# Performance work log

Hardware: AMD Instinct MI355X
Metric: run time of the kernel (lower is better)

## Reference

```python
import jax, jax.numpy as jnp
import numpy as np

TOL_A = 1e-09


def setup_inputs() -> dict:
    key = jax.random.key(0)
    ks = jax.random.split(key, 6)
    nx, nu, ny, bsz, T = 256, 128, 128, 128, 2048
    return {
        "u": jax.random.normal(ks[0], (bsz, T, nu), jnp.float32),
        "M": jax.random.normal(ks[1], (2 * nx, 2 * nx), jnp.float32),
        "B": jax.random.normal(ks[2], (nx, nu), jnp.float32),
        "C": jax.random.normal(ks[3], (ny, nx), jnp.float32),
        "D": jax.random.normal(ks[4], (ny, nu), jnp.float32),
        "x0": jax.random.normal(ks[5], (nx, 1), jnp.float32),
    }


def _compute_A(M):
    # LMI-based stable A: S = M M^T + tol*I; A = E^{-1} F
    nx = M.shape[0] // 2
    S = M @ M.T + TOL_A * jnp.eye(2 * nx, dtype=M.dtype)
    F = S[nx:, :nx]
    P = S[nx:, nx:]
    E = 0.5 * (P + S[:nx, :nx])
    return jnp.linalg.solve(E, F)  # == inv(E) @ F


def reference(u, M, B, C, D, x0):
    # u: (bsz, T, nu); returns predictions (bsz, T, ny)
    nx = B.shape[0]
    A = _compute_A(M)  # time-invariant: computed once instead of per step
    bsz = u.shape[0]
    x = jnp.broadcast_to(x0[:, 0], (bsz, nx))  # learned x0 stacked over batch
    # t=0 output: C x0 + D u_0 (faithful to torch code)
    y0 = x @ C.T + u[:, 0] @ D.T

    def step(x, u_t):
        # x_{t+1} = A x_t + B u_t ; y_{t+1} = C x_{t+1} + D u_t (off-by-one D term, as in source)
        x = x @ A.T + u_t @ B.T
        y = x @ C.T + u_t @ D.T
        return x, y

    # scan over time: xs is (T-1, bsz, nu)
    _, ys = jax.lax.scan(step, x, jnp.swapaxes(u[:, :-1], 0, 1))
    preds = jnp.concatenate([y0[None], ys], axis=0)  # (T, bsz, ny)
    return jnp.swapaxes(preds, 0, 1)
```

## Files before the change

### kernel.cpp

```cpp
#include <hip/hip_runtime.h>

#define NX 256
#define NU 128
#define NY 128
#define BSZ 128
#define TT 2048
#define LCH 32
#define KCH 64

typedef _Float16 h8 __attribute__((ext_vector_type(8)));
typedef _Float16 h4 __attribute__((ext_vector_type(4)));
typedef float f4 __attribute__((ext_vector_type(4)));

__device__ __forceinline__ f4 mfma16(h8 a, h8 b, f4 c) {
  return __builtin_amdgcn_mfma_f32_16x16x32_f16(a, b, c, 0, 0, 0);
}
#define PIN(x) asm volatile("" : "+v"(x))

__device__ __forceinline__ int swz256(int row, int bc) { return row * 256 + (bc ^ ((row & 7) << 4)); }

__device__ __forceinline__ h8 cvt8(f4 lo, f4 hi) {
  h8 h;
#pragma unroll
  for (int j = 0; j < 4; ++j) { h[j] = (_Float16)lo[j]; h[j + 4] = (_Float16)hi[j]; }
  return h;
}
__device__ __forceinline__ h4 h4cvt(f4 v) {
  h4 h;
#pragma unroll
  for (int j = 0; j < 4; ++j) h[j] = (_Float16)v[j];
  return h;
}
__device__ __forceinline__ h8 h8zero() {
  h8 h;
#pragma unroll
  for (int j = 0; j < 8; ++j) h[j] = (_Float16)0.0f;
  return h;
}

__device__ __forceinline__ void mm_core(const float* __restrict__ a, const float* __restrict__ b,
                                        int Nb, int i0, int j0, int tid,
                                        float (*As)[32][65], float (*Bs)[64][33],
                                        float acc[2][2]) {
  const int ar = tid >> 4, ac = (tid & 15) * 4;
  const int br = tid >> 3, bc = (tid & 7) * 4;
  const int tx = tid & 15, ty = tid >> 4;
  f4 pa0 = *(const f4*)(a + (size_t)(i0 + ar) * 256 + ac);
  f4 pa1 = *(const f4*)(a + (size_t)(i0 + ar + 16) * 256 + ac);
  f4 pb0 = *(const f4*)(b + (size_t)br * Nb + j0 + bc);
  f4 pb1 = *(const f4*)(b + (size_t)(br + 32) * Nb + j0 + bc);
  for (int r4 = 0; r4 < 4; ++r4) {
    const int bs = r4 & 1;
#pragma unroll
    for (int m = 0; m < 4; ++m) {
      As[bs][ar][ac + m] = pa0[m];
      As[bs][ar + 16][ac + m] = pa1[m];
      Bs[bs][br][bc + m] = pb0[m];
      Bs[bs][br + 32][bc + m] = pb1[m];
    }
    if (r4 < 3) {
      int kk = (r4 + 1) * 64;
      pa0 = *(const f4*)(a + (size_t)(i0 + ar) * 256 + kk + ac);
      pa1 = *(const f4*)(a + (size_t)(i0 + ar + 16) * 256 + kk + ac);
      pb0 = *(const f4*)(b + (size_t)(kk + br) * Nb + j0 + bc);
      pb1 = *(const f4*)(b + (size_t)(kk + br + 32) * Nb + j0 + bc);
    }
    __syncthreads();
#pragma unroll 8
    for (int k = 0; k < 64; ++k) {
      float a0 = As[bs][ty * 2][k], a1 = As[bs][ty * 2 + 1][k];
      float b0 = Bs[bs][k][tx * 2], b1 = Bs[bs][k][tx * 2 + 1];
      acc[0][0] += a0 * b0; acc[0][1] += a0 * b1;
      acc[1][0] += a1 * b0; acc[1][1] += a1 * b1;
    }
  }
}

__global__ __launch_bounds__(256) void k_ef(const float* __restrict__ M, const float* __restrict__ B,
                                            const float* __restrict__ C, const float* __restrict__ D,
                                            const float* __restrict__ x0, const float* __restrict__ u,
                                            float* __restrict__ E, float* __restrict__ F,
                                            _Float16* __restrict__ B16, float* __restrict__ out) {
  const int tid = threadIdx.x;
  int z = blockIdx.x >> 6;
  if (z >= 2) {
    if (blockIdx.x < 192) {
      int idx = (blockIdx.x - 128) * 256 + tid;
      int b = idx >> 7, col = idx & 127;
      const float* crow = C + (size_t)col * 256;
      const float* drow = D + (size_t)col * 128;
      const float* ur = u + (size_t)b * (TT * NU);
      float s = 0.f;
#pragma unroll 8
      for (int j = 0; j < 256; j += 4) {
        f4 cv = *(const f4*)(crow + j);
        f4 xv = *(const f4*)(x0 + j);
        s += cv[0] * xv[0] + cv[1] * xv[1] + cv[2] * xv[2] + cv[3] * xv[3];
      }
#pragma unroll 8
      for (int j = 0; j < 128; j += 4) {
        f4 dv = *(const f4*)(drow + j);
        f4 uv = *(const f4*)(ur + j);
        s += dv[0] * uv[0] + dv[1] * uv[1] + dv[2] * uv[2] + dv[3] * uv[3];
      }
      out[(size_t)b * (TT * NY) + col] = s;
    } else {
      int i = (blockIdx.x - 192) * 1024 + tid;
      B16[i] = (_Float16)B[i];
      B16[i + 256] = (_Float16)B[i + 256];
      B16[i + 512] = (_Float16)B[i + 512];
      B16[i + 768] = (_Float16)B[i + 768];
    }
    return;
  }
  __shared__ float Ps[2][32][65], Qs[2][32][65];
  int tile = blockIdx.x & 63;
  int i0 = (tile >> 3) * 32, j0 = (tile & 7) * 32;
  const int ar = tid >> 4, ac = (tid & 15) * 4;
  const int tx = tid & 15, ty = tid >> 4;
  float acc[2][2] = {{0.f, 0.f}, {0.f, 0.f}};
  int np = (z == 0) ? 2 : 1;
  int rc = 0;
  for (int p = 0; p < np; ++p) {
    int po = (z == 0) ? p * 256 : 256;
    int qo = (z == 0) ? p * 256 : 0;
    f4 p0 = *(const f4*)(M + (size_t)(i0 + po + ar) * 512 + ac);
    f4 p1 = *(const f4*)(M + (size_t)(i0 + po + ar + 16) * 512 + ac);
    f4 q0 = *(const f4*)(M + (size_t)(j0 + qo + ar) * 512 + ac);
    f4 q1 = *(const f4*)(M + (size_t)(j0 + qo + ar + 16) * 512 + ac);
    for (int kk = 0; kk < 512; kk += 64) {
      const int bs = rc & 1;
      ++rc;
#pragma unroll
      for (int m = 0; m < 4; ++m) {
        Ps[bs][ar][ac + m] = p0[m];
        Ps[bs][ar + 16][ac + m] = p1[m];
        Qs[bs][ar][ac + m] = q0[m];
        Qs[bs][ar + 16][ac + m] = q1[m];
      }
      if (kk < 448) {
        int k2 = kk + 64;
        p0 = *(const f4*)(M + (size_t)(i0 + po + ar) * 512 + k2 + ac);
        p1 = *(const f4*)(M + (size_t)(i0 + po + ar + 16) * 512 + k2 + ac);
        q0 = *(const f4*)(M + (size_t)(j0 + qo + ar) * 512 + k2 + ac);
        q1 = *(const f4*)(M + (size_t)(j0 + qo + ar + 16) * 512 + k2 + ac);
      }
      __syncthreads();
#pragma unroll 8
      for (int k = 0; k < 64; ++k) {
        float a0 = Ps[bs][ty * 2][k], a1 = Ps[bs][ty * 2 + 1][k];
        float b0 = Qs[bs][tx * 2][k], b1 = Qs[bs][tx * 2 + 1][k];
        acc[0][0] += a0 * b0; acc[0][1] += a0 * b1;
        acc[1][0] += a1 * b0; acc[1][1] += a1 * b1;
      }
    }
  }
#pragma unroll
  for (int ii = 0; ii < 2; ++ii)
#pragma unroll
    for (int jj = 0; jj < 2; ++jj) {
      int i = i0 + ty * 2 + ii, j = j0 + tx * 2 + jj;
      if (z == 0) {
        float v = 0.5f * acc[ii][jj];
        if (i == j) v += 1e-9f;
        E[i * 256 + j] = v;
      } else {
        F[i * 256 + j] = acc[ii][jj];
      }
    }
}

__global__ __launch_bounds__(256) void k_ns0(const float* __restrict__ E,
                                             float* __restrict__ X, float* __restrict__ Y) {
  __shared__ float As[2][32][65];
  __shared__ float Bs[2][64][33];
  __shared__ float s1[256], red[256];
  const int tid = threadIdx.x;
  {
    float s = 0.f;
    const float* row = E + (size_t)tid * 256;
#pragma unroll 8
    for (int j = 0; j < 256; j += 4) {
      f4 e = *(const f4*)(row + j);
      s += e[0] + e[1] + e[2] + e[3];
    }
    s1[tid] = s; red[tid] = s * s;
  }
  __syncthreads();
  for (int o = 128; o > 0; o >>= 1) { if (tid < o) red[tid] += red[tid + o]; __syncthreads(); }
  float n1 = red[0];
  __syncthreads();
  {
    float s = 0.f;
    const float* row = E + (size_t)tid * 256;
#pragma unroll 8
    for (int j = 0; j < 256; j += 4) {
      f4 e = *(const f4*)(row + j);
      f4 vv = *(const f4*)(&s1[j]);
      s += e[0] * vv[0] + e[1] * vv[1] + e[2] * vv[2] + e[3] * vv[3];
    }
    red[tid] = s * s;
  }
  __syncthreads();
  for (int o = 128; o > 0; o >>= 1) { if (tid < o) red[tid] += red[tid + o]; __syncthreads(); }
  float c = sqrtf(n1 / red[0]);
  __syncthreads();
  if (blockIdx.x < 64) {
    int i0 = (blockIdx.x >> 3) * 32, j0 = (blockIdx.x & 7) * 32;
    float acc[2][2] = {{0.f, 0.f}, {0.f, 0.f}};
    mm_core(E, E, 256, i0, j0, tid, As, Bs, acc);
    int tx = tid & 15, ty = tid >> 4;
#pragma unroll
    for (int ii = 0; ii < 2; ++ii)
#pragma unroll
      for (int jj = 0; jj < 2; ++jj) {
        int i = i0 + ty * 2 + ii, j = j0 + tx * 2 + jj;
        Y[(size_t)i * 256 + j] = 2.f * c * E[(size_t)i * 256 + j] - c * c * acc[ii][jj];
      }
  } else {
    int idx = (blockIdx.x - 64) * 1024 + tid * 4;
    int i = idx >> 8, j = idx & 255;
    f4 e = *(const f4*)(E + idx);
    f4 v;
#pragma unroll
    for (int m = 0; m < 4; ++m) v[m] = ((j + m) == i ? 2.f * c : 0.f) - c * c * e[m];
    *(f4*)(X + idx) = v;
  }
}

struct MMJob {
  const float* a; const float* b; const float* add;
  float* d32; _Float16* d16;
  int M, N, mode, blk0;
};

__global__ __launch_bounds__(256) void k_mm(MMJob j0, MMJob j1, MMJob j2, int njobs) {
  __shared__ float As[2][32][65];
  __shared__ float Bs[2][64][33];
  const int tid = threadIdx.x;
  int bid = blockIdx.x;
  MMJob jb = j0;
  if (njobs > 1 && bid >= j1.blk0) jb = j1;
  if (njobs > 2 && bid >= j2.blk0) jb = j2;
  int rel = bid - jb.blk0;
  int ntile = jb.N >> 5;
  int i0 = (rel / ntile) * 32, j0g = (rel % ntile) * 32;
  float acc[2][2] = {{0.f, 0.f}, {0.f, 0.f}};
  mm_core(jb.a, jb.b, jb.N, i0, j0g, tid, As, Bs, acc);
  int tx = tid & 15, ty = tid >> 4;
#pragma unroll
  for (int ii = 0; ii < 2; ++ii)
#pragma unroll
    for (int jj = 0; jj < 2; ++jj) {
      int i = i0 + ty * 2 + ii, j = j0g + tx * 2 + jj;
      size_t o = (size_t)i * jb.N + j;
      float v = acc[ii][jj];
      if (jb.mode == 1) v = 2.f * jb.a[(size_t)i * 256 + j] - v;
      else if (jb.add) v += jb.add[o];
      if (jb.d32) jb.d32[o] = v;
      if (jb.d16) jb.d16[o] = (_Float16)v;
    }
}

__global__ __launch_bounds__(512, 2) void k_recW(const float* __restrict__ u,
                                                 const _Float16* __restrict__ A16,
                                                 const _Float16* __restrict__ B16,
                                                 float* __restrict__ w) {
  __shared__ __align__(16) char sm[24576];
  char* xb = sm;
  char* ub = sm + 16384;
  const int tid = threadIdx.x, lane = tid & 63, wv = tid >> 6;
  const int g = lane >> 4, lr = lane & 15;
  const int chunk = blockIdx.x >> 3, btile = blockIdx.x & 7;
  const int b0 = btile * 16, t0 = chunk * LCH, nt0 = wv * 2;

  h8 Ar[2][8], Bf[2][4];
#pragma unroll
  for (int n2 = 0; n2 < 2; ++n2) {
#pragma unroll
    for (int kf = 0; kf < 8; ++kf) {
      Ar[n2][kf] = *(const h8*)(A16 + (size_t)((nt0 + n2) * 16 + lr) * NX + kf * 32 + g * 8);
      PIN(Ar[n2][kf]);
    }
#pragma unroll
    for (int kf = 0; kf < 4; ++kf) {
      Bf[n2][kf] = *(const h8*)(B16 + (size_t)((nt0 + n2) * 16 + lr) * NU + kf * 32 + g * 8);
      PIN(Bf[n2][kf]);
    }
  }
  const int urow = tid >> 5, uuc = tid & 31;
  const float* ubase = u + (size_t)(b0 + urow) * (TT * NU) + uuc * 4;
  const int uoff = swz256(urow, uuc * 8);
  {
    f4 r0 = *(const f4*)(ubase + (size_t)t0 * NU);
    *(h4*)(ub + uoff) = h4cvt(r0);
  }
  f4 urA = *(const f4*)(ubase + (size_t)(t0 + 1) * NU);
  f4 urB = *(const f4*)(ubase + (size_t)(t0 + 2 < TT ? t0 + 2 : TT - 1) * NU);
  h8 af[8];
#pragma unroll
  for (int kf = 0; kf < 8; ++kf) af[kf] = h8zero();
  __syncthreads();

  f4 z4 = {0.f, 0.f, 0.f, 0.f};
  f4 xacc[2];
#pragma unroll 2
  for (int i = 0; i < LCH; ++i) {
    const int p = i & 1;
    if (i < LCH - 1) {
      int nt = t0 + i + 3;
      if (nt > TT - 1) nt = TT - 1;
      if (p == 0) {
        *(h4*)(ub + 4096 + uoff) = h4cvt(urA);
        urA = *(const f4*)(ubase + (size_t)nt * NU);
      } else {
        *(h4*)(ub + uoff) = h4cvt(urB);
        urB = *(const f4*)(ubase + (size_t)nt * NU);
      }
    }
    h8 uf[4];
#pragma unroll
    for (int kf = 0; kf < 4; ++kf)
      uf[kf] = *(const h8*)(ub + p * 4096 + swz256(lr, kf * 64 + g * 16));
    __builtin_amdgcn_s_setprio(1);
    xacc[0] = z4; xacc[1] = z4;
#pragma unroll
    for (int kf = 0; kf < 8; ++kf) {
      xacc[0] = mfma16(Ar[0][kf], af[kf], xacc[0]);
      xacc[1] = mfma16(Ar[1][kf], af[kf], xacc[1]);
    }
#pragma unroll
    for (int kf = 0; kf < 4; ++kf) {
      xacc[0] = mfma16(Bf[0][kf], uf[kf], xacc[0]);
      xacc[1] = mfma16(Bf[1][kf], uf[kf], xacc[1]);
    }
    __builtin_amdgcn_s_setprio(0);
    if (i < LCH - 1) {
#pragma unroll
      for (int n2 = 0; n2 < 2; ++n2)
        *(h4*)(xb + (p ^ 1) * 8192 + lr * 512 + ((((nt0 + n2) * 32) + g * 8) ^ ((lr & 7) << 4))) =
            h4cvt(xacc[n2]);
      __syncthreads();
#pragma unroll
      for (int kf = 0; kf < 8; ++kf)
        af[kf] = *(const h8*)(xb + (p ^ 1) * 8192 + lr * 512 + ((kf * 64 + g * 16) ^ ((lr & 7) << 4)));
    }
  }
#pragma unroll
  for (int n2 = 0; n2 < 2; ++n2)
    *(f4*)(w + ((size_t)chunk * BSZ + b0 + lr) * NX + (nt0 + n2) * 16 + g * 4) = xacc[n2];
}

__global__ __launch_bounds__(512, 2) void k_phB(const float* __restrict__ x0,
                                                const float* __restrict__ w,
                                                const _Float16* __restrict__ Ah16,
                                                float* __restrict__ xs) {
  __shared__ __align__(16) char xb[16384];
  const int tid = threadIdx.x, lane = tid & 63, wv = tid >> 6;
  const int g = lane >> 4, lr = lane & 15;
  const int b0 = blockIdx.x * 16, nt0 = wv * 2;
  h8 Ar[2][8];
#pragma unroll
  for (int n2 = 0; n2 < 2; ++n2)
#pragma unroll
    for (int kf = 0; kf < 8; ++kf) {
      Ar[n2][kf] = *(const h8*)(Ah16 + (size_t)((nt0 + n2) * 16 + lr) * NX + kf * 32 + g * 8);
      PIN(Ar[n2][kf]);
    }
  for (int s = 0; s < 8; ++s) {
    int e = tid + s * 512;
    int row = e >> 8, c = e & 255;
    xs[(size_t)(b0 + row) * NX + c] = x0[c];
  }
  h8 af[8];
#pragma unroll
  for (int kf = 0; kf < 8; ++kf) {
    const float* sp = x0 + kf * 32 + g * 8;
    af[kf] = cvt8(*(const f4*)sp, *(const f4*)(sp + 4));
  }
  f4 wl[2];
#pragma unroll
  for (int n2 = 0; n2 < 2; ++n2)
    wl[n2] = *(const f4*)(w + ((size_t)0 * BSZ + b0 + lr) * NX + (nt0 + n2) * 16 + g * 4);
  f4 z4 = {0.f, 0.f, 0.f, 0.f};
  for (int k = 0; k < KCH - 1; ++k) {
    const int p = k & 1;
    f4 wn[2] = {z4, z4};
    if (k < KCH - 2) {
#pragma unroll
      for (int n2 = 0; n2 < 2; ++n2)
        wn[n2] = *(const f4*)(w + ((size_t)(k + 1) * BSZ + b0 + lr) * NX + (nt0 + n2) * 16 + g * 4);
    }
    f4 acc[2] = {z4, z4};
#pragma unroll
    for (int kf = 0; kf < 8; ++kf) {
      acc[0] = mfma16(Ar[0][kf], af[kf], acc[0]);
      acc[1] = mfma16(Ar[1][kf], af[kf], acc[1]);
    }
#pragma unroll
    for (int n2 = 0; n2 < 2; ++n2) {
      acc[n2] += wl[n2];
      *(f4*)(xs + ((size_t)(k + 1) * BSZ + b0 + lr) * NX + (nt0 + n2) * 16 + g * 4) = acc[n2];
    }
    if (k < KCH - 2) {
#pragma unroll
      for (int n2 = 0; n2 < 2; ++n2)
        *(h4*)(xb + (p ^ 1) * 8192 + lr * 512 + ((((nt0 + n2) * 32) + g * 8) ^ ((lr & 7) << 4))) =
            h4cvt(acc[n2]);
      __syncthreads();
#pragma unroll
      for (int kf = 0; kf < 8; ++kf)
        af[kf] = *(const h8*)(xb + (p ^ 1) * 8192 + lr * 512 + ((kf * 64 + g * 16) ^ ((lr & 7) << 4)));
    }
#pragma unroll
    for (int n2 = 0; n2 < 2; ++n2) wl[n2] = wn[n2];
  }
}

__global__ __launch_bounds__(512, 2) void k_recY(const float* __restrict__ u,
                                                 const _Float16* __restrict__ A16,
                                                 const _Float16* __restrict__ B16,
                                                 const _Float16* __restrict__ CA16,
                                                 const _Float16* __restrict__ CBD16,
                                                 const float* __restrict__ xs,
                                                 float* __restrict__ out) {
  __shared__ __align__(16) char sm[24576];
  char* xb = sm;
  char* ub = sm + 16384;
  const int tid = threadIdx.x, lane = tid & 63, wv = tid >> 6;
  const int g = lane >> 4, lr = lane & 15;
  const int chunk = blockIdx.x >> 3, btile = blockIdx.x & 7;
  const int b0 = btile * 16, t0 = chunk * LCH, nt0 = wv * 2;

  h8 Ar[2][8], Bf[2][4], Cf[8], Df[4];
#pragma unroll
  for (int n2 = 0; n2 < 2; ++n2) {
#pragma unroll
    for (int kf = 0; kf < 8; ++kf) {
      Ar[n2][kf] = *(const h8*)(A16 + (size_t)((nt0 + n2) * 16 + lr) * NX + kf * 32 + g * 8);
      PIN(Ar[n2][kf]);
    }
#pragma unroll
    for (int kf = 0; kf < 4; ++kf) {
      Bf[n2][kf] = *(const h8*)(B16 + (size_t)((nt0 + n2) * 16 + lr) * NU + kf * 32 + g * 8);
      PIN(Bf[n2][kf]);
    }
  }
#pragma unroll
  for (int kf = 0; kf < 8; ++kf) {
    Cf[kf] = *(const h8*)(CA16 + (size_t)(wv * 16 + lr) * NX + kf * 32 + g * 8);
    PIN(Cf[kf]);
  }
#pragma unroll
  for (int kf = 0; kf < 4; ++kf) {
    Df[kf] = *(const h8*)(CBD16 + (size_t)(wv * 16 + lr) * NU + kf * 32 + g * 8);
    PIN(Df[kf]);
  }
  h8 af[8];
#pragma unroll
  for (int kf = 0; kf < 8; ++kf) {
    const float* sp = xs + ((size_t)chunk * BSZ + b0 + lr) * NX + kf * 32 + g * 8;
    af[kf] = cvt8(*(const f4*)sp, *(const f4*)(sp + 4));
  }
  const int urow = tid >> 5, uuc = tid & 31;
  const float* ubase = u + (size_t)(b0 + urow) * (TT * NU) + uuc * 4;
  const int uoff = swz256(urow, uuc * 8);
  float* obase = out + (size_t)(b0 + lr) * (TT * NY) + wv * 16 + g * 4;
  {
    f4 r0 = *(const f4*)(ubase + (size_t)t0 * NU);
    *(h4*)(ub + uoff) = h4cvt(r0);
  }
  f4 urA = *(const f4*)(ubase + (size_t)(t0 + 1) * NU);
  f4 urB = *(const f4*)(ubase + (size_t)(t0 + 2 < TT ? t0 + 2 : TT - 1) * NU);
  __syncthreads();

  f4 z4 = {0.f, 0.f, 0.f, 0.f};
#pragma unroll 2
  for (int i = 0; i < LCH; ++i) {
    const int p = i & 1;
    if (i < LCH - 1) {
      int nt = t0 + i + 3;
      if (nt > TT - 1) nt = TT - 1;
      if (p == 0) {
        *(h4*)(ub + 4096 + uoff) = h4cvt(urA);
        urA = *(const f4*)(ubase + (size_t)nt * NU);
      } else {
        *(h4*)(ub + uoff) = h4cvt(urB);
        urB = *(const f4*)(ubase + (size_t)nt * NU);
      }
    }
    h8 uf[4];
#pragma unroll
    for (int kf = 0; kf < 4; ++kf)
      uf[kf] = *(const h8*)(ub + p * 4096 + swz256(lr, kf * 64 + g * 16));
    __builtin_amdgcn_s_setprio(1);
    f4 yacc = z4;
#pragma unroll
    for (int kf = 0; kf < 8; ++kf) yacc = mfma16(Cf[kf], af[kf], yacc);
#pragma unroll
    for (int kf = 0; kf < 4; ++kf) yacc = mfma16(Df[kf], uf[kf], yacc);
    __builtin_amdgcn_s_setprio(0);
    int t = t0 + i + 1;
    if (t < TT) *(f4*)(obase + (size_t)t * NY) = yacc;
    if (i < LCH - 1) {
      __builtin_amdgcn_s_setprio(1);
      f4 xacc[2] = {z4, z4};
#pragma unroll
      for (int kf = 0; kf < 8; ++kf) {
        xacc[0] = mfma16(Ar[0][kf], af[kf], xacc[0]);
        xacc[1] = mfma16(Ar[1][kf], af[kf], xacc[1]);
      }
#pragma unroll
      for (int kf = 0; kf < 4; ++kf) {
        xacc[0] = mfma16(Bf[0][kf], uf[kf], xacc[0]);
        xacc[1] = mfma16(Bf[1][kf], uf[kf], xacc[1]);
      }
      __builtin_amdgcn_s_setprio(0);
#pragma unroll
      for (int n2 = 0; n2 < 2; ++n2)
        *(h4*)(xb + (p ^ 1) * 8192 + lr * 512 + ((((nt0 + n2) * 32) + g * 8) ^ ((lr & 7) << 4))) =
            h4cvt(xacc[n2]);
      __syncthreads();
#pragma unroll
      for (int kf = 0; kf < 8; ++kf)
        af[kf] = *(const h8*)(xb + (p ^ 1) * 8192 + lr * 512 + ((kf * 64 + g * 16) ^ ((lr & 7) << 4)));
    }
  }
}

extern "C" void kernel_launch(void* const* d_in, const int* in_sizes, int n_in,
                              void* d_out, int out_size, void* d_ws, size_t ws_size,
                              hipStream_t stream) {
  const float* u  = (const float*)d_in[0];
  const float* M  = (const float*)d_in[1];
  const float* B  = (const float*)d_in[2];
  const float* C  = (const float*)d_in[3];
  const float* D  = (const float*)d_in[4];
  const float* x0 = (const float*)d_in[5];
  float* out = (float*)d_out;
  char* ws = (char*)d_ws;

  float* E    = (float*)(ws + 0L);
  float* F    = (float*)(ws + 256L * 1024);
  float* X1   = (float*)(ws + 512L * 1024);
  float* Y1   = (float*)(ws + 768L * 1024);
  float* X2   = (float*)(ws + 1024L * 1024);
  float* Y2   = (float*)(ws + 1280L * 1024);
  float* Amat = (float*)(ws + 1536L * 1024);
  float* P2   = (float*)(ws + 1792L * 1024);
  float* P4   = (float*)(ws + 2048L * 1024);
  float* P8   = (float*)(ws + 2304L * 1024);
  float* P16  = (float*)(ws + 2560L * 1024);
  _Float16* A16   = (_Float16*)(ws + 2816L * 1024);
  _Float16* Ah16  = (_Float16*)(ws + 2944L * 1024);
  _Float16* B16   = (_Float16*)(ws + 3072L * 1024);
  _Float16* CA16  = (_Float16*)(ws + 3136L * 1024);
  _Float16* CBD16 = (_Float16*)(ws + 3200L * 1024);
  float* wbuf = (float*)(ws + 9408L * 1024);
  float* xs   = (float*)(ws + 17600L * 1024);

  MMJob nil = {nullptr, nullptr, nullptr, nullptr, nullptr, 0, 0, 0, 0};

  k_ef<<<224, 256, 0, stream>>>(M, B, C, D, x0, u, E, F, B16, out);
  k_ns0<<<128, 256, 0, stream>>>(E, X1, Y1);
  float *Xc = X1, *Yc = Y1, *Xn = X2, *Yn = Y2;
  for (int it = 0; it < 8; ++it) {
    MMJob jx = {Xc, Yc, nullptr, Xn, nullptr, 256, 256, 1, 0};
    MMJob jy = {Yc, Yc, nullptr, Yn, nullptr, 256, 256, 1, 64};
    k_mm<<<128, 256, 0, stream>>>(jx, jy, nil, 2);
    float* t1 = Xc; Xc = Xn; Xn = t1;
    float* t2 = Yc; Yc = Yn; Yn = t2;
  }
  {
    MMJob ja = {Xc, F, nullptr, Amat, A16, 256, 256, 0, 0};
    k_mm<<<64, 256, 0, stream>>>(ja, nil, nil, 1);
  }
  {
    MMJob j0 = {Amat, Amat, nullptr, P2, nullptr, 256, 256, 0, 0};
    MMJob j1 = {C, Amat, nullptr, nullptr, CA16, 128, 256, 0, 64};
    MMJob j2 = {C, B, D, nullptr, CBD16, 128, 128, 0, 96};
    k_mm<<<112, 256, 0, stream>>>(j0, j1, j2, 3);
  }
  {
    MMJob j0 = {P2, P2, nullptr, P4, nullptr, 256, 256, 0, 0};
    k_mm<<<64, 256, 0, stream>>>(j0, nil, nil, 1);
  }
  {
    MMJob j0 = {P4, P4, nullptr, P8, nullptr, 256, 256, 0, 0};
    k_mm<<<64, 256, 0, stream>>>(j0, nil, nil, 1);
  }
  {
    MMJob j0 = {P8, P8, nullptr, P16, nullptr, 256, 256, 0, 0};
    k_mm<<<64, 256, 0, stream>>>(j0, nil, nil, 1);
  }
  {
    MMJob j0 = {P16, P16, nullptr, nullptr, Ah16, 256, 256, 0, 0};
    k_mm<<<64, 256, 0, stream>>>(j0, nil, nil, 1);
  }

  k_recW<<<512, 512, 0, stream>>>(u, A16, B16, wbuf);
  k_phB<<<8, 512, 0, stream>>>(x0, wbuf, Ah16, xs);
  k_recY<<<512, 512, 0, stream>>>(u, A16, B16, CA16, CBD16, xs, out);
}
```

Baseline: 368.6 us.

## Fuse setup matmul chain into persistent kernel with grid barriers; lighten recurrence barriers

Replaces the Newton-Schulz iteration launch and the sequence of small matmul launches (A, A powers, C*A, C*B+D) with one persistent 128-block kernel that uses an atomic-counter grid barrier between stages. The counter is zeroed in the preceding kernel. This removes roughly fifteen kernel launch gaps. In the recurrence kernels, __syncthreads is replaced by an LDS-only waitcnt plus barrier, and in k_recY the next-state MFMA is moved ahead of the output computation so the barrier covers less work. Risks: the grid barrier assumes all 128 blocks are co-resident, and spinning on atomics adds some latency.

Measured after the change: 668.3 us. +81.3%, slower.

```diff
diff --git a/kernel.cpp b/kernel.cpp
--- a/kernel.cpp
+++ b/kernel.cpp
@@ -7,6 +7,7 @@
 #define TT 2048
 #define LCH 32
 #define KCH 64
+#define NSB 128
 
 typedef _Float16 h8 __attribute__((ext_vector_type(8)));
 typedef _Float16 h4 __attribute__((ext_vector_type(4)));
@@ -16,6 +17,7 @@
   return __builtin_amdgcn_mfma_f32_16x16x32_f16(a, b, c, 0, 0, 0);
 }
 #define PIN(x) asm volatile("" : "+v"(x))
+#define LBAR() asm volatile("s_waitcnt lgkmcnt(0)\n\ts_barrier" ::: "memory")
 
 __device__ __forceinline__ int swz256(int row, int bc) { return row * 256 + (bc ^ ((row & 7) << 4)); }
 
@@ -80,8 +82,10 @@
                                             const float* __restrict__ C, const float* __restrict__ D,
                                             const float* __restrict__ x0, const float* __restrict__ u,
                                             float* __restrict__ E, float* __restrict__ F,
-                                            _Float16* __restrict__ B16, float* __restrict__ out) {
+                                            _Float16* __restrict__ B16, float* __restrict__ out,
+                                            int* __restrict__ cnt) {
   const int tid = threadIdx.x;
+  if (blockIdx.x == 0 && tid == 0) *cnt = 0;
   int z = blockIdx.x >> 6;
   if (z >= 2) {
     if (blockIdx.x < 192) {
@@ -170,96 +174,175 @@
     }
 }
 
-__global__ __launch_bounds__(256) void k_ns0(const float* __restrict__ E,
-                                             float* __restrict__ X, float* __restrict__ Y) {
+struct SP2 {
+  const float *Cm, *Bm, *Dm;
+  float *E, *F, *X1, *Y1, *X2, *Y2, *Am, *P2m, *P4m, *P8m, *P16m;
+  _Float16 *A16, *Ah16, *CA16, *CBD16;
+  int* cnt;
+};
+
+__device__ __forceinline__ void gbar(int* cnt, int target) {
+  __syncthreads();
+  __threadfence();
+  if (threadIdx.x == 0) {
+    atomicAdd(cnt, 1);
+    while (atomicAdd(cnt, 0) < target) __builtin_amdgcn_s_sleep(1);
+  }
+  __syncthreads();
+  __threadfence();
+}
+
+__global__ __launch_bounds__(256, 1) void k_setup2(SP2 P) {
   __shared__ float As[2][32][65];
   __shared__ float Bs[2][64][33];
-  __shared__ float s1[256], red[256];
-  const int tid = threadIdx.x;
+  const int bid = blockIdx.x, tid = threadIdx.x;
+  const int tx = tid & 15, ty = tid >> 4;
+  int bar = 0;
+
+  float c;
   {
-    float s = 0.f;
-    const float* row = E + (size_t)tid * 256;
+    float* s1 = &As[0][0][0];
+    float* red = s1 + 256;
+    {
+      float s = 0.f;
+      const float* row = P.E + (size_t)tid * 256;
 #pragma unroll 8
-    for (int j = 0; j < 256; j += 4) {
-      f4 e = *(const f4*)(row + j);
-      s += e[0] + e[1] + e[2] + e[3];
-    }
-    s1[tid] = s; red[tid] = s * s;
-  }
-  __syncthreads();
-  for (int o = 128; o > 0; o >>= 1) { if (tid < o) red[tid] += red[tid + o]; __syncthreads(); }
-  float n1 = red[0];
-  __syncthreads();
-  {
-    float s = 0.f;
-    const float* row = E + (size_t)tid * 256;
+      for (int j = 0; j < 256; j += 4) {
+        f4 e = *(const f4*)(row + j);
+        s += e[0] + e[1] + e[2] + e[3];
+      }
+      s1[tid] = s; red[tid] = s * s;
+    }
+    __syncthreads();
+    for (int o = 128; o > 0; o >>= 1) { if (tid < o) red[tid] += red[tid + o]; __syncthreads(); }
+    float n1 = red[0];
+    __syncthreads();
+    {
+      float s = 0.f;
+      const float* row = P.E + (size_t)tid * 256;
 #pragma unroll 8
-    for (int j = 0; j < 256; j += 4) {
-      f4 e = *(const f4*)(row + j);
-      f4 vv = *(const f4*)(&s1[j]);
-      s += e[0] * vv[0] + e[1] * vv[1] + e[2] * vv[2] + e[3] * vv[3];
-    }
-    red[tid] = s * s;
-  }
-  __syncthreads();
-  for (int o = 128; o > 0; o >>= 1) { if (tid < o) red[tid] += red[tid + o]; __syncthreads(); }
-  float c = sqrtf(n1 / red[0]);
-  __syncthreads();
-  if (blockIdx.x < 64) {
-    int i0 = (blockIdx.x >> 3) * 32, j0 = (blockIdx.x & 7) * 32;
+      for (int j = 0; j < 256; j += 4) {
+        f4 e = *(const f4*)(row + j);
+        f4 vv = *(const f4*)(&s1[j]);
+        s += e[0] * vv[0] + e[1] * vv[1] + e[2] * vv[2] + e[3] * vv[3];
+      }
+      red[tid] = s * s;
+    }
+    __syncthreads();
+    for (int o = 128; o > 0; o >>= 1) { if (tid < o) red[tid] += red[tid + o]; __syncthreads(); }
+    c = sqrtf(n1 / red[0]);
+    __syncthreads();
+  }
+  if (bid < 64) {
+    int i0 = (bid >> 3) * 32, j0 = (bid & 7) * 32;
     float acc[2][2] = {{0.f, 0.f}, {0.f, 0.f}};
-    mm_core(E, E, 256, i0, j0, tid, As, Bs, acc);
-    int tx = tid & 15, ty = tid >> 4;
+    mm_core(P.E, P.E, 256, i0, j0, tid, As, Bs, acc);
 #pragma unroll
     for (int ii = 0; ii < 2; ++ii)
 #pragma unroll
       for (int jj = 0; jj < 2; ++jj) {
         int i = i0 + ty * 2 + ii, j = j0 + tx * 2 + jj;
-        Y[(size_t)i * 256 + j] = 2.f * c * E[(size_t)i * 256 + j] - c * c * acc[ii][jj];
+        P.Y1[(size_t)i * 256 + j] = 2.f * c * P.E[(size_t)i * 256 + j] - c * c * acc[ii][jj];
       }
   } else {
-    int idx = (blockIdx.x - 64) * 1024 + tid * 4;
+    int idx = (bid - 64) * 1024 + tid * 4;
     int i = idx >> 8, j = idx & 255;
-    f4 e = *(const f4*)(E + idx);
+    f4 e = *(const f4*)(P.E + idx);
     f4 v;
 #pragma unroll
     for (int m = 0; m < 4; ++m) v[m] = ((j + m) == i ? 2.f * c : 0.f) - c * c * e[m];
-    *(f4*)(X + idx) = v;
-  }
-}
-
-struct MMJob {
-  const float* a; const float* b; const float* add;
-  float* d32; _Float16* d16;
-  int M, N, mode, blk0;
-};
-
-__global__ __launch_bounds__(256) void k_mm(MMJob j0, MMJob j1, MMJob j2, int njobs) {
-  __shared__ float As[2][32][65];
-  __shared__ float Bs[2][64][33];
-  const int tid = threadIdx.x;
-  int bid = blockIdx.x;
-  MMJob jb = j0;
-  if (njobs > 1 && bid >= j1.blk0) jb = j1;
-  if (njobs > 2 && bid >= j2.blk0) jb = j2;
-  int rel = bid - jb.blk0;
-  int ntile = jb.N >> 5;
-  int i0 = (rel / ntile) * 32, j0g = (rel % ntile) * 32;
-  float acc[2][2] = {{0.f, 0.f}, {0.f, 0.f}};
-  mm_core(jb.a, jb.b, jb.N, i0, j0g, tid, As, Bs, acc);
-  int tx = tid & 15, ty = tid >> 4;
-#pragma unroll
-  for (int ii = 0; ii < 2; ++ii)
-#pragma unroll
-    for (int jj = 0; jj < 2; ++jj) {
-      int i = i0 + ty * 2 + ii, j = j0g + tx * 2 + jj;
-      size_t o = (size_t)i * jb.N + j;
-      float v = acc[ii][jj];
-      if (jb.mode == 1) v = 2.f * jb.a[(size_t)i * 256 + j] - v;
-      else if (jb.add) v += jb.add[o];
-      if (jb.d32) jb.d32[o] = v;
-      if (jb.d16) jb.d16[o] = (_Float16)v;
-    }
+    *(f4*)(P.X1 + idx) = v;
+  }
+  gbar(P.cnt, NSB * ++bar);
+
+  float *Xc = P.X1, *Yc = P.Y1, *Xn = P.X2, *Yn = P.Y2;
+  for (int it = 0; it < 8; ++it) {
+    const float* a = (bid < 64) ? Xc : Yc;
+    float* d = (bid < 64) ? Xn : Yn;
+    int t2 = bid & 63;
+    int i0 = (t2 >> 3) * 32, j0 = (t2 & 7) * 32;
+    float acc[2][2] = {{0.f, 0.f}, {0.f, 0.f}};
+    mm_core(a, Yc, 256, i0, j0, tid, As, Bs, acc);
+#pragma unroll
+    for (int ii = 0; ii < 2; ++ii)
+#pragma unroll
+      for (int jj = 0; jj < 2; ++jj) {
+        int i = i0 + ty * 2 + ii, j = j0 + tx * 2 + jj;
+        d[(size_t)i * 256 + j] = 2.f * a[(size_t)i * 256 + j] - acc[ii][jj];
+      }
+    gbar(P.cnt, NSB * ++bar);
+    float* s;
+    s = Xc; Xc = Xn; Xn = s;
+    s = Yc; Yc = Yn; Yn = s;
+  }
+
+  if (bid < 64) {
+    int i0 = (bid >> 3) * 32, j0 = (bid & 7) * 32;
+    float acc[2][2] = {{0.f, 0.f}, {0.f, 0.f}};
+    mm_core(Xc, P.F, 256, i0, j0, tid, As, Bs, acc);
+#pragma unroll
+    for (int ii = 0; ii < 2; ++ii)
+#pragma unroll
+      for (int jj = 0; jj < 2; ++jj) {
+        int i = i0 + ty * 2 + ii, j = j0 + tx * 2 + jj;
+        P.Am[(size_t)i * 256 + j] = acc[ii][jj];
+        P.A16[(size_t)i * 256 + j] = (_Float16)acc[ii][jj];
+      }
+  }
+  gbar(P.cnt, NSB * ++bar);
+
+  if (bid < 64) {
+    int i0 = (bid >> 3) * 32, j0 = (bid & 7) * 32;
+    float acc[2][2] = {{0.f, 0.f}, {0.f, 0.f}};
+    mm_core(P.Am, P.Am, 256, i0, j0, tid, As, Bs, acc);
+#pragma unroll
+    for (int ii = 0; ii < 2; ++ii)
+#pragma unroll
+      for (int jj = 0; jj < 2; ++jj)
+        P.P2m[(size_t)(i0 + ty * 2 + ii) * 256 + j0 + tx * 2 + jj] = acc[ii][jj];
+  } else if (bid < 96) {
+    int rt = bid - 64;
+    int i0 = (rt >> 3) * 32, j0 = (rt & 7) * 32;
+    float acc[2][2] = {{0.f, 0.f}, {0.f, 0.f}};
+    mm_core(P.Cm, P.Am, 256, i0, j0, tid, As, Bs, acc);
+#pragma unroll
+    for (int ii = 0; ii < 2; ++ii)
+#pragma unroll
+      for (int jj = 0; jj < 2; ++jj)
+        P.CA16[(size_t)(i0 + ty * 2 + ii) * 256 + j0 + tx * 2 + jj] = (_Float16)acc[ii][jj];
+  } else if (bid < 112) {
+    int rt = bid - 96;
+    int i0 = (rt >> 2) * 32, j0 = (rt & 3) * 32;
+    float acc[2][2] = {{0.f, 0.f}, {0.f, 0.f}};
+    mm_core(P.Cm, P.Bm, 128, i0, j0, tid, As, Bs, acc);
+#pragma unroll
+    for (int ii = 0; ii < 2; ++ii)
+#pragma unroll
+      for (int jj = 0; jj < 2; ++jj) {
+        int i = i0 + ty * 2 + ii, j = j0 + tx * 2 + jj;
+        P.CBD16[(size_t)i * 128 + j] = (_Float16)(acc[ii][jj] + P.Dm[(size_t)i * 128 + j]);
+      }
+  }
+  gbar(P.cnt, NSB * ++bar);
+
+  const float* pw_src[4] = {P.P2m, P.P4m, P.P8m, P.P16m};
+  float* pw_dst[3] = {P.P4m, P.P8m, P.P16m};
+  for (int s = 0; s < 4; ++s) {
+    if (bid < 64) {
+      int i0 = (bid >> 3) * 32, j0 = (bid & 7) * 32;
+      float acc[2][2] = {{0.f, 0.f}, {0.f, 0.f}};
+      mm_core(pw_src[s], pw_src[s], 256, i0, j0, tid, As, Bs, acc);
+#pragma unroll
+      for (int ii = 0; ii < 2; ++ii)
+#pragma unroll
+        for (int jj = 0; jj < 2; ++jj) {
+          int i = i0 + ty * 2 + ii, j = j0 + tx * 2 + jj;
+          if (s < 3) pw_dst[s][(size_t)i * 256 + j] = acc[ii][jj];
+          else P.Ah16[(size_t)i * 256 + j] = (_Float16)acc[ii][jj];
+        }
+    }
+    if (s < 3) gbar(P.cnt, NSB * ++bar);
+  }
 }
 
 __global__ __launch_bounds__(512, 2) void k_recW(const float* __restrict__ u,
@@ -340,7 +423,7 @@
       for (int n2 = 0; n2 < 2; ++n2)
         *(h4*)(xb + (p ^ 1) * 8192 + lr * 512 + ((((nt0 + n2) * 32) + g * 8) ^ ((lr & 7) << 4))) =
             h4cvt(xacc[n2]);
-      __syncthreads();
+      LBAR();
 #pragma unroll
       for (int kf = 0; kf < 8; ++kf)
         af[kf] = *(const h8*)(xb + (p ^ 1) * 8192 + lr * 512 + ((kf * 64 + g * 16) ^ ((lr & 7) << 4)));
@@ -407,7 +490,7 @@
       for (int n2 = 0; n2 < 2; ++n2)
         *(h4*)(xb + (p ^ 1) * 8192 + lr * 512 + ((((nt0 + n2) * 32) + g * 8) ^ ((lr & 7) << 4))) =
             h4cvt(acc[n2]);
-      __syncthreads();
+      LBAR();
 #pragma unroll
       for (int kf = 0; kf < 8; ++kf)
         af[kf] = *(const h8*)(xb + (p ^ 1) * 8192 + lr * 512 + ((kf * 64 + g * 16) ^ ((lr & 7) << 4)));
@@ -493,6 +576,25 @@
 #pragma unroll
     for (int kf = 0; kf < 4; ++kf)
       uf[kf] = *(const h8*)(ub + p * 4096 + swz256(lr, kf * 64 + g * 16));
+    if (i < LCH - 1) {
+      __builtin_amdgcn_s_setprio(1);
+      f4 xacc[2] = {z4, z4};
+#pragma unroll
+      for (int kf = 0; kf < 8; ++kf) {
+        xacc[0] = mfma16(Ar[0][kf], af[kf], xacc[0]);
+        xacc[1] = mfma16(Ar[1][kf], af[kf], xacc[1]);
+      }
+#pragma unroll
+      for (int kf = 0; kf < 4; ++kf) {
+        xacc[0] = mfma16(Bf[0][kf], uf[kf], xacc[0]);
+        xacc[1] = mfma16(Bf[1][kf], uf[kf], xacc[1]);
+      }
+      __builtin_amdgcn_s_setprio(0);
+#pragma unroll
+      for (int n2 = 0; n2 < 2; ++n2)
+        *(h4*)(xb + (p ^ 1) * 8192 + lr * 512 + ((((nt0 + n2) * 32) + g * 8) ^ ((lr & 7) << 4))) =
+            h4cvt(xacc[n2]);
+    }
     __builtin_amdgcn_s_setprio(1);
     f4 yacc = z4;
 #pragma unroll
@@ -503,24 +605,7 @@
     int t = t0 + i + 1;
     if (t < TT) *(f4*)(obase + (size_t)t * NY) = yacc;
     if (i < LCH - 1) {
-      __builtin_amdgcn_s_setprio(1);
-      f4 xacc[2] = {z4, z4};
-#pragma unroll
-      for (int kf = 0; kf < 8; ++kf) {
-        xacc[0] = mfma16(Ar[0][kf], af[kf], xacc[0]);
-        xacc[1] = mfma16(Ar[1][kf], af[kf], xacc[1]);
-      }
-#pragma unroll
-      for (int kf = 0; kf < 4; ++kf) {
-        xacc[0] = mfma16(Bf[0][kf], uf[kf], xacc[0]);
-        xacc[1] = mfma16(Bf[1][kf], uf[kf], xacc[1]);
-      }
-      __builtin_amdgcn_s_setprio(0);
-#pragma unroll
-      for (int n2 = 0; n2 < 2; ++n2)
-        *(h4*)(xb + (p ^ 1) * 8192 + lr * 512 + ((((nt0 + n2) * 32) + g * 8) ^ ((lr & 7) << 4))) =
-            h4cvt(xacc[n2]);
-      __syncthreads();
+      LBAR();
 #pragma unroll
       for (int kf = 0; kf < 8; ++kf)
         af[kf] = *(const h8*)(xb + (p ^ 1) * 8192 + lr * 512 + ((kf * 64 + g * 16) ^ ((lr & 7) << 4)));
@@ -556,48 +641,14 @@
   _Float16* B16   = (_Float16*)(ws + 3072L * 1024);
   _Float16* CA16  = (_Float16*)(ws + 3136L * 1024);
   _Float16* CBD16 = (_Float16*)(ws + 3200L * 1024);
+  int* cnt = (int*)(ws + 4096L * 1024);
   float* wbuf = (float*)(ws + 9408L * 1024);
   float* xs   = (float*)(ws + 17600L * 1024);
 
-  MMJob nil = {nullptr, nullptr, nullptr, nullptr, nullptr, 0, 0, 0, 0};
-
-  k_ef<<<224, 256, 0, stream>>>(M, B, C, D, x0, u, E, F, B16, out);
-  k_ns0<<<128, 256, 0, stream>>>(E, X1, Y1);
-  float *Xc = X1, *Yc = Y1, *Xn = X2, *Yn = Y2;
-  for (int it = 0; it < 8; ++it) {
-    MMJob jx = {Xc, Yc, nullptr, Xn, nullptr, 256, 256, 1, 0};
-    MMJob jy = {Yc, Yc, nullptr, Yn, nullptr, 256, 256, 1, 64};
-    k_mm<<<128, 256, 0, stream>>>(jx, jy, nil, 2);
-    float* t1 = Xc; Xc = Xn; Xn = t1;
-    float* t2 = Yc; Yc = Yn; Yn = t2;
-  }
-  {
-    MMJob ja = {Xc, F, nullptr, Amat, A16, 256, 256, 0, 0};
-    k_mm<<<64, 256, 0, stream>>>(ja, nil, nil, 1);
-  }
-  {
-    MMJob j0 = {Amat, Amat, nullptr, P2, nullptr, 256, 256, 0, 0};
-    MMJob j1 = {C, Amat, nullptr, nullptr, CA16, 128, 256, 0, 64};
-    MMJob j2 = {C, B, D, nullptr, CBD16, 128, 128, 0, 96};
-    k_mm<<<112, 256, 0, stream>>>(j0, j1, j2, 3);
-  }
-  {
-    MMJob j0 = {P2, P2, nullptr, P4, nullptr, 256, 256, 0, 0};
-    k_mm<<<64, 256, 0, stream>>>(j0, nil, nil, 1);
-  }
-  {
-    MMJob j0 = {P4, P4, nullptr, P8, nullptr, 256, 256, 0, 0};
-    k_mm<<<64, 256, 0, stream>>>(j0, nil, nil, 1);
-  }
-  {
-    MMJob j0 = {P8, P8, nullptr, P16, nullptr, 256, 256, 0, 0};
-    k_mm<<<64, 256, 0, stream>>>(j0, nil, nil, 1);
-  }
-  {
-    MMJob j0 = {P16, P16, nullptr, nullptr, Ah16, 256, 256, 0, 0};
-    k_mm<<<64, 256, 0, stream>>>(j0, nil, nil, 1);
-  }
-
+  k_ef<<<224, 256, 0, stream>>>(M, B, C, D, x0, u, E, F, B16, out, cnt);
+  SP2 sp = {C, B, D, E, F, X1, Y1, X2, Y2, Amat, P2, P4, P8, P16,
+            A16, Ah16, CA16, CBD16, cnt};
+  k_setup2<<<128, 256, 0, stream>>>(sp);
   k_recW<<<512, 512, 0, stream>>>(u, A16, B16, wbuf);
   k_phB<<<8, 512, 0, stream>>>(x0, wbuf, Ah16, xs);
   k_recY<<<512, 512, 0, stream>>>(u, A16, B16, CA16, CBD16, xs, out);
```
